# Performance work log

Measured on AMD Instinct MI355X. Metric: run time of the kernel, lower is better.

Reference implementation:

```python
import jax, jax.numpy as jnp
import numpy as np

B, T, D = 1, 1024, 4096
H, HK, DH = 32, 8, 128          # n_heads, n_kv_heads, head_dim
N_REP = H // HK                 # GQA repeat factor
RQ, RKV, RO, RFF = 64, 64, 1024, 1024
INTER = 14336
EPS = 1e-5
THETA = 10000.0


def _rms_norm(x, w):
    # LLaMA RMSNorm: x * rsqrt(mean(x^2)+eps) * w
    var = jnp.mean(x * x, axis=-1, keepdims=True)
    return x * jax.lax.rsqrt(var + EPS) * w


def _rope_cos_sin(t_len, dh):
    # _SimpleRoPE semantics: interleaved repeat of angles (repeat_interleave(2))
    evens = jnp.arange(0, dh, 2, dtype=jnp.float32)
    inv = 1.0 / (THETA ** (evens / dh))                 # [dh/2]
    t = jnp.arange(t_len, dtype=jnp.float32)
    ang = t[:, None] * inv[None, :]                     # [T, dh/2]
    ang = jnp.repeat(ang, 2, axis=-1)                   # [T, dh]
    return jnp.cos(ang), jnp.sin(ang)


def _rotate_half(x):
    # HF rotate_half: split in half along last dim
    half = x.shape[-1] // 2
    return jnp.concatenate([-x[..., half:], x[..., :half]], axis=-1)


def _apply_rope(q, k, cos, sin):
    # q,k: [B,H,T,dh]; cos/sin: [T,dh] broadcast over B,H
    c = cos[None, None]
    s = sin[None, None]
    return q * c + _rotate_half(q) * s, k * c + _rotate_half(k) * s


def _proj_per_head(x, Us, V):
    # x: [B,T,D], V: [h,r,D], Us: [h,dh,r] -> [B,h,T,dh]
    xr = jnp.einsum('btd,hrd->bthr', x, V)
    return jnp.einsum('bthr,hdr->bhtd', xr, Us)


def setup_inputs() -> dict:
    key = jax.random.key(0)
    ks = jax.random.split(key, 16)
    sc = 0.02
    inp = {
        'hidden_states': jax.random.normal(ks[0], (B, T, D), jnp.float32),
        'ln1_w': jnp.ones((D,), jnp.float32),
        'ln2_w': jnp.ones((D,), jnp.float32),
        'q_Us': jax.random.normal(ks[1], (H, DH, RQ), jnp.float32) * sc,
        'q_V': jax.random.normal(ks[2], (H, RQ, D), jnp.float32) * sc,
        'k_Us': jax.random.normal(ks[3], (HK, DH, RKV), jnp.float32) * sc,
        'k_V': jax.random.normal(ks[4], (HK, RKV, D), jnp.float32) * sc,
        'v_Us': jax.random.normal(ks[5], (HK, DH, RKV), jnp.float32) * sc,
        'v_V': jax.random.normal(ks[6], (HK, RKV, D), jnp.float32) * sc,
        'o_Us': jax.random.normal(ks[7], (D, RO), jnp.float32) * sc,
        'o_V': jax.random.normal(ks[8], (RO, H * DH), jnp.float32) * sc,
        'g_Us': jax.random.normal(ks[9], (INTER, RFF), jnp.float32) * sc,
        'g_V': jax.random.normal(ks[10], (RFF, D), jnp.float32) * sc,
        'u_Us': jax.random.normal(ks[11], (INTER, RFF), jnp.float32) * sc,
        'u_V': jax.random.normal(ks[12], (RFF, D), jnp.float32) * sc,
        'd_Us': jax.random.normal(ks[13], (D, RFF), jnp.float32) * sc,
        'd_V': jax.random.normal(ks[14], (RFF, INTER), jnp.float32) * sc,
    }
    return inp


def reference(hidden_states, ln1_w, ln2_w, q_Us, q_V, k_Us, k_V, v_Us, v_V,
              o_Us, o_V, g_Us, g_V, u_Us, u_V, d_Us, d_V):
    x = hidden_states
    # --- attention ---
    h1 = _rms_norm(x, ln1_w)
    q = _proj_per_head(h1, q_Us, q_V)            # [B,H,T,dh]
    k = _proj_per_head(h1, k_Us, k_V)            # [B,HK,T,dh]
    v = _proj_per_head(h1, v_Us, v_V)            # [B,HK,T,dh]
    cos, sin = _rope_cos_sin(T, DH)
    q, k = _apply_rope(q, k, cos, sin)
    k = jnp.repeat(k, N_REP, axis=1)             # GQA expand -> [B,H,T,dh]
    v = jnp.repeat(v, N_REP, axis=1)
    scale = 1.0 / np.sqrt(DH)
    scores = jnp.einsum('bhtd,bhsd->bhts', q, k) * scale   # [B,H,T,T]
    causal = jnp.tril(jnp.ones((T, T), bool))
    scores = jnp.where(causal[None, None], scores, jnp.float32(-1e30))
    p = jax.nn.softmax(scores, axis=-1)
    attn = jnp.einsum('bhts,bhsd->bhtd', p, v)   # [B,H,T,dh]
    attn = attn.transpose(0, 2, 1, 3).reshape(B, T, H * DH)
    # low-rank o: y = attn @ W_o^T = (attn @ V^T) @ Us^T
    y = jnp.einsum('btr,dr->btd', jnp.einsum('bte,re->btr', attn, o_V), o_Us)
    x = x + y
    # --- SwiGLU MLP with low-rank factors ---
    h2 = _rms_norm(x, ln2_w)
    g = jnp.einsum('btr,ir->bti', jnp.einsum('btd,rd->btr', h2, g_V), g_Us)
    u = jnp.einsum('btr,ir->bti', jnp.einsum('btd,rd->btr', h2, u_V), u_Us)
    hmid = jax.nn.silu(g) * u                    # [B,T,INTER]
    dn = jnp.einsum('btr,dr->btd', jnp.einsum('bti,ri->btr', hmid, d_V), d_Us)
    return x + dn
```

## Files before the change

### kernel.cpp

```cpp
#include <hip/hip_runtime.h>
#include <math.h>


typedef __bf16 bf16;
typedef __bf16 bf16x8 __attribute__((ext_vector_type(8)));
typedef __bf16 bf16x4 __attribute__((ext_vector_type(4)));
typedef float  f32x4  __attribute__((ext_vector_type(4)));

#define EPI_BF16   0
#define EPI_BF16T  1
#define EPI_F32ADD 2
#define EPI_SILU1  3
#define EPI_MUL    4
#define EPI_PART   5

__device__ __forceinline__ void gld16(const void* g, void* l) {
    __builtin_amdgcn_global_load_lds(
        (const __attribute__((address_space(1))) unsigned int*)g,
        (__attribute__((address_space(3))) unsigned int*)l, 16, 0, 0);
}

template<int EPI>
__global__ __launch_bounds__(256)
void gemm3f(const bf16* __restrict__ A, int lda, long sA,
            const float* __restrict__ B, int ldb, long sB, const float* __restrict__ B2,
            void* __restrict__ Cv, int ldc, long sC,
            const float* __restrict__ R, int Kc, int nsplit, int gx)
{
    __shared__ __align__(16) bf16  As[128 * 64];
    __shared__ __align__(16) float Bs[128 * 64];

    const int tid = threadIdx.x, lane = tid & 63, w = tid >> 6;
    const int wr = w >> 1, wc = w & 1;

    int id = blockIdx.x;
    {
        const int nwg = gridDim.x;
        int q = nwg >> 3, rr = nwg & 7;
        int xcd = id & 7, off = id >> 3;
        id = (xcd < rr ? xcd * (q + 1) : rr * (q + 1) + (xcd - rr) * q) + off;
    }
    const int bm = id % gx, bn = id / gx, bz = blockIdx.z;
    const int ks = bz % nsplit, zb = bz / nsplit;

    const float* Bp = (B2 != nullptr && zb != 0) ? B2 : B;
    const bf16*  Ab = A  + (long)zb * sA + (long)(bm * 128) * lda + (long)ks * Kc;
    const float* Bb = Bp + (long)zb * sB + (long)(bn * 128) * ldb + (long)ks * Kc;

    const int g = lane >> 4, r = lane & 15;
    f32x4 acc[4][4] = {};
    const int nt = Kc >> 6;

    for (int t = 0; t < nt; t++) {
        if (t) __syncthreads();
        const bf16*  At = Ab + t * 64;
        const float* Bt = Bb + t * 64;
        #pragma unroll
        for (int i = 0; i < 4; i++) {
            int cb = w * 256 + i * 64, ci = cb + lane;
            int row = ci >> 3, col = ((ci & 7) ^ (row & 7)) * 8;
            gld16(At + (long)row * lda + col, &As[cb * 8]);
        }
        #pragma unroll
        for (int i = 0; i < 8; i++) {
            int cb = w * 512 + i * 64, ci = cb + lane;
            int row = ci >> 4, col = ((ci & 15) ^ (row & 15)) * 4;
            gld16(Bt + (long)row * ldb + col, &Bs[cb * 4]);
        }
        __syncthreads();
        #pragma unroll
        for (int kk = 0; kk < 2; kk++) {
            bf16x8 af[4], bfr[4];
            #pragma unroll
            for (int m = 0; m < 4; m++) {
                int row = wr * 64 + m * 16 + r;
                af[m] = *(const bf16x8*)&As[row * 64 + (((kk * 4 + g) ^ (row & 7)) * 8)];
            }
            #pragma unroll
            for (int n = 0; n < 4; n++) {
                int row = wc * 64 + n * 16 + r;
                int c0 = kk * 8 + g * 2;
                f32x4 lo = *(const f32x4*)&Bs[row * 64 + (((c0    ) ^ (row & 15)) * 4)];
                f32x4 hi = *(const f32x4*)&Bs[row * 64 + (((c0 + 1) ^ (row & 15)) * 4)];
                bfr[n] = bf16x8{(bf16)lo[0], (bf16)lo[1], (bf16)lo[2], (bf16)lo[3],
                                (bf16)hi[0], (bf16)hi[1], (bf16)hi[2], (bf16)hi[3]};
            }
            #pragma unroll
            for (int m = 0; m < 4; m++)
                #pragma unroll
                for (int n = 0; n < 4; n++)
                    acc[m][n] = __builtin_amdgcn_mfma_f32_16x16x32_bf16(af[m], bfr[n], acc[m][n], 0, 0, 0);
        }
    }

    #pragma unroll
    for (int m = 0; m < 4; m++) {
        #pragma unroll
        for (int n = 0; n < 4; n++) {
            const int row0 = bm * 128 + wr * 64 + m * 16 + g * 4;
            const int col  = bn * 128 + wc * 64 + n * 16 + r;
            #pragma unroll
            for (int j = 0; j < 4; j++) {
                float v = acc[m][n][j];
                long row = row0 + j;
                if constexpr (EPI == EPI_BF16) {
                    ((bf16*)Cv)[(long)zb * sC + row * (long)ldc + col] = (bf16)v;
                } else if constexpr (EPI == EPI_BF16T) {
                    ((bf16*)Cv)[(long)zb * sC + (long)col * ldc + row] = (bf16)v;
                } else if constexpr (EPI == EPI_F32ADD) {
                    long idx = row * (long)ldc + col;
                    ((float*)Cv)[idx] = v + R[idx];
                } else if constexpr (EPI == EPI_PART) {
                    ((float*)Cv)[(long)bz * sC + row * (long)ldc + col] = v;
                } else if constexpr (EPI == EPI_SILU1) {
                    ((bf16*)Cv)[row * (long)ldc + col] = (bf16)(v / (1.f + __expf(-v)));
                } else {
                    bf16* p = &((bf16*)Cv)[row * (long)ldc + col];
                    *p = (bf16)((float)*p * v);
                }
            }
        }
    }
}

template<int EPI>
__global__ __launch_bounds__(256)
void gemm2(const bf16* __restrict__ A, int lda, long sA,
           const float* __restrict__ B, int ldb, long sB, const float* __restrict__ B2,
           void* __restrict__ Cv, int ldc, long sC,
           const float* __restrict__ R, int Kc, int nsplit)
{
    __shared__ __align__(16) bf16 As[2][128 * 64];
    __shared__ __align__(16) bf16 Bs[2][128 * 64];

    const int tid = threadIdx.x, lane = tid & 63, w = tid >> 6;
    const int wr = w >> 1, wc = w & 1;
    const int bm = blockIdx.x, bn = blockIdx.y, bz = blockIdx.z;
    const int ks = bz % nsplit, zb = bz / nsplit;

    const float* Bp = (B2 != nullptr && zb != 0) ? B2 : B;
    const bf16*  Ab = A  + (long)zb * sA + (long)(bm * 128) * lda + (long)ks * Kc;
    const float* Bb = Bp + (long)zb * sB + (long)(bn * 128) * ldb + (long)ks * Kc;

    const int g = lane >> 4, r = lane & 15;
    f32x4 acc[4][4] = {};
    const int nt = Kc >> 6;
    int cur = 0;

    {
        #pragma unroll
        for (int i = 0; i < 4; i++) {
            int cb = i * 256 + w * 64, ci = cb + lane;
            int arow = ci >> 3, acol = ((ci & 7) ^ (arow & 7)) * 8;
            gld16(Ab + (long)arow * lda + acol, &As[0][cb * 8]);
        }
        float4 fb[8];
        #pragma unroll
        for (int i = 0; i < 8; i++) {
            int p = i * 256 + tid;
            fb[i] = *(const float4*)(Bb + (long)(p >> 4) * ldb + (p & 15) * 4);
        }
        #pragma unroll
        for (int i = 0; i < 8; i++) {
            int p = i * 256 + tid, brow = p >> 4, c4 = p & 15;
            bf16x4 h = {(bf16)fb[i].x, (bf16)fb[i].y, (bf16)fb[i].z, (bf16)fb[i].w};
            *(bf16x4*)&Bs[0][brow * 64 + (((c4 >> 1) ^ (brow & 7)) * 8) + (c4 & 1) * 4] = h;
        }
    }
    __syncthreads();

    for (int t = 0; t < nt; t++) {
        float4 fb[8];
        if (t + 1 < nt) {
            const bf16* An = Ab + (t + 1) * 64;
            #pragma unroll
            for (int i = 0; i < 4; i++) {
                int cb = i * 256 + w * 64, ci = cb + lane;
                int arow = ci >> 3, acol = ((ci & 7) ^ (arow & 7)) * 8;
                gld16(An + (long)arow * lda + acol, &As[cur ^ 1][cb * 8]);
            }
            const float* Bn = Bb + (t + 1) * 64;
            #pragma unroll
            for (int i = 0; i < 8; i++) {
                int p = i * 256 + tid;
                fb[i] = *(const float4*)(Bn + (long)(p >> 4) * ldb + (p & 15) * 4);
            }
        }
        #pragma unroll
        for (int kk = 0; kk < 2; kk++) {
            bf16x8 af[4], bfr[4];
            #pragma unroll
            for (int m = 0; m < 4; m++) {
                int row = wr * 64 + m * 16 + r;
                af[m] = *(const bf16x8*)&As[cur][row * 64 + (((kk * 4 + g) ^ (row & 7)) * 8)];
            }
            #pragma unroll
            for (int n = 0; n < 4; n++) {
                int row = wc * 64 + n * 16 + r;
                bfr[n] = *(const bf16x8*)&Bs[cur][row * 64 + (((kk * 4 + g) ^ (row & 7)) * 8)];
            }
            #pragma unroll
            for (int m = 0; m < 4; m++)
                #pragma unroll
                for (int n = 0; n < 4; n++)
                    acc[m][n] = __builtin_amdgcn_mfma_f32_16x16x32_bf16(af[m], bfr[n], acc[m][n], 0, 0, 0);
        }
        if (t + 1 < nt) {
            #pragma unroll
            for (int i = 0; i < 8; i++) {
                int p = i * 256 + tid, brow = p >> 4, c4 = p & 15;
                bf16x4 h = {(bf16)fb[i].x, (bf16)fb[i].y, (bf16)fb[i].z, (bf16)fb[i].w};
                *(bf16x4*)&Bs[cur ^ 1][brow * 64 + (((c4 >> 1) ^ (brow & 7)) * 8) + (c4 & 1) * 4] = h;
            }
            __syncthreads();
            cur ^= 1;
        }
    }

    #pragma unroll
    for (int m = 0; m < 4; m++) {
        #pragma unroll
        for (int n = 0; n < 4; n++) {
            const int row0 = bm * 128 + wr * 64 + m * 16 + g * 4;
            const int col  = bn * 128 + wc * 64 + n * 16 + r;
            #pragma unroll
            for (int j = 0; j < 4; j++) {
                float v = acc[m][n][j];
                long row = row0 + j;
                if constexpr (EPI == EPI_BF16) {
                    ((bf16*)Cv)[(long)zb * sC + row * (long)ldc + col] = (bf16)v;
                } else if constexpr (EPI == EPI_BF16T) {
                    ((bf16*)Cv)[(long)zb * sC + (long)col * ldc + row] = (bf16)v;
                } else if constexpr (EPI == EPI_F32ADD) {
                    long idx = row * (long)ldc + col;
                    ((float*)Cv)[idx] = v + R[idx];
                } else if constexpr (EPI == EPI_PART) {
                    ((float*)Cv)[(long)bz * sC + row * (long)ldc + col] = v;
                } else if constexpr (EPI == EPI_SILU1) {
                    ((bf16*)Cv)[row * (long)ldc + col] = (bf16)(v / (1.f + __expf(-v)));
                } else {
                    bf16* p = &((bf16*)Cv)[row * (long)ldc + col];
                    *p = (bf16)((float)*p * v);
                }
            }
        }
    }
}

__global__ __launch_bounds__(256)
void reduce_k(const float* __restrict__ part, long pe, int np, bf16* __restrict__ out)
{
    long i = ((long)blockIdx.x * 256 + threadIdx.x) * 4;
    float4 s = *(const float4*)&part[i];
    for (int p = 1; p < np; p++) {
        float4 v = *(const float4*)&part[(long)p * pe + i];
        s.x += v.x; s.y += v.y; s.z += v.z; s.w += v.w;
    }
    bf16x4 o = {(bf16)s.x, (bf16)s.y, (bf16)s.z, (bf16)s.w};
    *(bf16x4*)&out[i] = o;
}

__global__ __launch_bounds__(256)
void rmsnorm_k(const float* __restrict__ x, const float* __restrict__ w,
               bf16* __restrict__ out)
{
    const int D = 4096;
    const long row = blockIdx.x;
    const float* xr = x + row * D;
    float4 v[4];
    float ss = 0.f;
    #pragma unroll
    for (int k = 0; k < 4; k++) {
        v[k] = *(const float4*)&xr[threadIdx.x * 4 + k * 1024];
        ss += v[k].x * v[k].x + v[k].y * v[k].y + v[k].z * v[k].z + v[k].w * v[k].w;
    }
    #pragma unroll
    for (int o = 32; o > 0; o >>= 1) ss += __shfl_down(ss, o);
    __shared__ float red[4];
    if ((threadIdx.x & 63) == 0) red[threadIdx.x >> 6] = ss;
    __syncthreads();
    float rs = rsqrtf((red[0] + red[1] + red[2] + red[3]) / D + 1e-5f);
    #pragma unroll
    for (int k = 0; k < 4; k++) {
        int i = threadIdx.x * 4 + k * 1024;
        float4 wv = *(const float4*)&w[i];
        bf16x4 o4 = {(bf16)(v[k].x * rs * wv.x), (bf16)(v[k].y * rs * wv.y),
                     (bf16)(v[k].z * rs * wv.z), (bf16)(v[k].w * rs * wv.w)};
        *(bf16x4*)&out[row * D + i] = o4;
    }
}

__global__ __launch_bounds__(256)
void rope_table_k(float* cs, float* sn)
{
    int idx = blockIdx.x * blockDim.x + threadIdx.x;
    int t = idx >> 6, i = idx & 63;
    float inv = powf(10000.0f, -(2.0f * i) / 128.0f);
    float a = (float)t * inv;
    cs[idx] = cosf(a);
    sn[idx] = sinf(a);
}

__global__ __launch_bounds__(256)
void rope_k(bf16* qk, const float* __restrict__ cs, const float* __restrict__ sn)
{
    long idx = (long)blockIdx.x * blockDim.x + threadIdx.x;
    int d = idx & 63;
    long ht = idx >> 6;
    int t = (int)(ht & 1023);
    bf16* p = qk + ht * 128;
    float x1 = (float)p[d], x2 = (float)p[d + 64];
    int i1 = d >> 1;
    float c1 = cs[t * 64 + i1],      s1 = sn[t * 64 + i1];
    float c2 = cs[t * 64 + 32 + i1], s2 = sn[t * 64 + 32 + i1];
    p[d]      = (bf16)(x1 * c1 - x2 * s1);
    p[d + 64] = (bf16)(x2 * c2 + x1 * s2);
}

__global__ __launch_bounds__(256)
void attn_k(const bf16* __restrict__ Q,
            const bf16* __restrict__ Kb,
            const bf16* __restrict__ Vt,
            bf16* __restrict__ O)
{
    const int T = 1024;
    __shared__ __align__(16) bf16 Ks[64][128];
    __shared__ __align__(16) bf16 Vs[128][64];
    __shared__ __align__(16) bf16 Ps[4][16][72];

    const int qt = blockIdx.x, h = blockIdx.y, hk = h >> 2;
    const int tid = threadIdx.x, lane = tid & 63, w = tid >> 6;
    const int g = lane >> 4, r = lane & 15;
    const int qrow0 = qt * 64 + w * 16;

    bf16x8 qf[4];
    const bf16* qp = Q + ((long)h * T + qrow0 + r) * 128;
    #pragma unroll
    for (int dc = 0; dc < 4; dc++) qf[dc] = *(const bf16x8*)(qp + dc * 32 + g * 8);

    f32x4 o_acc[8] = {};
    float m_run[4], l_run[4];
    #pragma unroll
    for (int j = 0; j < 4; j++) { m_run[j] = -1e30f; l_run[j] = 0.f; }

    const float scale = 0.08838834764831845f;
    const int kv_end = qt * 64 + 64;

    for (int kv0 = 0; kv0 < kv_end; kv0 += 64) {
        __syncthreads();
        {
            int tr = tid >> 2;
            const bf16* src = Kb + ((long)hk * T + kv0 + tr) * 128;
            #pragma unroll
            for (int q4 = 0; q4 < 4; q4++) {
                int c = (tid & 3) * 4 + q4;
                bf16x8 v = *(const bf16x8*)(src + c * 8);
                *(bf16x8*)&Ks[tr][(c ^ (tr & 7)) * 8] = v;
            }
        }
        {
            int dd = tid >> 1;
            const bf16* src = Vt + ((long)hk * 128 + dd) * T + kv0;
            #pragma unroll
            for (int q4 = 0; q4 < 4; q4++) {
                int c = (tid & 1) * 4 + q4;
                bf16x8 v = *(const bf16x8*)(src + c * 8);
                *(bf16x8*)&Vs[dd][(c ^ (dd & 7)) * 8] = v;
            }
        }
        __syncthreads();

        f32x4 s[4] = {};
        #pragma unroll
        for (int n = 0; n < 4; n++) {
            int tr = n * 16 + r;
            #pragma unroll
            for (int dc = 0; dc < 4; dc++) {
                int c = (dc * 4 + g) ^ (tr & 7);
                bf16x8 kf = *(const bf16x8*)&Ks[tr][c * 8];
                s[n] = __builtin_amdgcn_mfma_f32_16x16x32_bf16(qf[dc], kf, s[n], 0, 0, 0);
            }
        }

        #pragma unroll
        for (int j = 0; j < 4; j++) {
            int qpos = qrow0 + g * 4 + j;
            float mx = m_run[j];
            #pragma unroll
            for (int n = 0; n < 4; n++) {
                int kpos = kv0 + n * 16 + r;
                float sv = s[n][j] * scale;
                sv = (kpos <= qpos) ? sv : -1e30f;
                s[n][j] = sv;
                mx = fmaxf(mx, sv);
            }
            #pragma unroll
            for (int mask = 1; mask < 16; mask <<= 1) mx = fmaxf(mx, __shfl_xor(mx, mask));
            float corr = __expf(m_run[j] - mx);
            l_run[j] *= corr;
            #pragma unroll
            for (int db = 0; db < 8; db++) o_acc[db][j] *= corr;
            float ls = 0.f;
            #pragma unroll
            for (int n = 0; n < 4; n++) {
                float p = __expf(s[n][j] - mx);
                s[n][j] = p;
                ls += p;
            }
            #pragma unroll
            for (int mask = 1; mask < 16; mask <<= 1) ls += __shfl_xor(ls, mask);
            l_run[j] += ls;
            m_run[j] = mx;
        }

        #pragma unroll
        for (int n = 0; n < 4; n++)
            #pragma unroll
            for (int j = 0; j < 4; j++)
                Ps[w][g * 4 + j][n * 16 + r] = (bf16)s[n][j];
        __syncthreads();

        bf16x8 pf[2];
        #pragma unroll
        for (int kc = 0; kc < 2; kc++)
            pf[kc] = *(const bf16x8*)&Ps[w][r][kc * 32 + g * 8];
        #pragma unroll
        for (int db = 0; db < 8; db++) {
            #pragma unroll
            for (int kc = 0; kc < 2; kc++) {
                int dd = db * 16 + r;
                int c = (kc * 4 + g) ^ (dd & 7);
                bf16x8 vf = *(const bf16x8*)&Vs[dd][c * 8];
                o_acc[db] = __builtin_amdgcn_mfma_f32_16x16x32_bf16(pf[kc], vf, o_acc[db], 0, 0, 0);
            }
        }
    }

    #pragma unroll
    for (int db = 0; db < 8; db++) {
        #pragma unroll
        for (int j = 0; j < 4; j++) {
            int t = qrow0 + g * 4 + j;
            float v = o_acc[db][j] / l_run[j];
            O[(long)t * 4096 + h * 128 + db * 16 + r] = (bf16)v;
        }
    }
}

extern "C" void kernel_launch(void* const* d_in, const int* in_sizes, int n_in,
                              void* d_out, int out_size, void* d_ws, size_t ws_size,
                              hipStream_t stream)
{
    const float* X   = (const float*)d_in[0];
    const float* LN1 = (const float*)d_in[1];
    const float* LN2 = (const float*)d_in[2];
    const float* qUs = (const float*)d_in[3];
    const float* qV  = (const float*)d_in[4];
    const float* kUs = (const float*)d_in[5];
    const float* kV  = (const float*)d_in[6];
    const float* vUs = (const float*)d_in[7];
    const float* vV  = (const float*)d_in[8];
    const float* oUs = (const float*)d_in[9];
    const float* oV  = (const float*)d_in[10];
    const float* gUs = (const float*)d_in[11];
    const float* gV  = (const float*)d_in[12];
    const float* uUs = (const float*)d_in[13];
    const float* uV  = (const float*)d_in[14];
    const float* dUs = (const float*)d_in[15];
    const float* dV  = (const float*)d_in[16];
    float* OUT = (float*)d_out;

    char* w = (char*)d_ws;
    bf16*  h1   = (bf16*)(w + 0);
    bf16*  xrq  = (bf16*)(w + 8388608);
    bf16*  xrk  = (bf16*)(w + 12582912);
    bf16*  xrv  = (bf16*)(w + 13631488);
    bf16*  qb   = (bf16*)(w + 14680064);
    bf16*  kb   = (bf16*)(w + 23068672);
    bf16*  vt   = (bf16*)(w + 25165824);
    float* cs   = (float*)(w + 27262976);
    float* sn   = (float*)(w + 27525120);
    bf16*  att  = (bf16*)(w + 27787264);
    bf16*  r1   = (bf16*)(w + 36175872);
    bf16*  h2   = (bf16*)(w + 0);
    bf16*  gr   = (bf16*)(w + 8388608);
    bf16*  ur   = (bf16*)(w + 10485760);
    bf16*  hmid = (bf16*)(w + 12582912);
    bf16*  dr   = (bf16*)(w + 41943040);
    const size_t ARENA  = 44040192;
    const size_t PARTSZ = 33554432;
    float* part = (float*)(w + ARENA);
    const bool med = ws_size >= ARENA + PARTSZ;

    dim3 blk(256);

    if (med) {
        rmsnorm_k<<<1024, blk, 0, stream>>>(X, LN1, h1);
        gemm3f<EPI_PART><<<dim3(128,1,4), blk, 0, stream>>>(h1,4096,0, qV,4096,0,nullptr, part,2048,2097152, nullptr, 1024,4, 8);
        reduce_k<<<2048, blk, 0, stream>>>(part, 2097152, 4, xrq);
        gemm3f<EPI_PART><<<dim3(32,1,8), blk, 0, stream>>>(h1,4096,0, kV,4096,0,vV, part,512,524288, nullptr, 1024,4, 8);
        reduce_k<<<512, blk, 0, stream>>>(part,             524288, 4, xrk);
        reduce_k<<<512, blk, 0, stream>>>(part + 4L*524288, 524288, 4, xrv);

        gemm3f<EPI_BF16 ><<<dim3(8,1,32), blk, 0, stream>>>(xrq,2048,64, qUs,64,8192,nullptr, qb,128,131072, nullptr, 64,1, 8);
        gemm3f<EPI_BF16 ><<<dim3(8,1, 8), blk, 0, stream>>>(xrk, 512,64, kUs,64,8192,nullptr, kb,128,131072, nullptr, 64,1, 8);
        gemm3f<EPI_BF16T><<<dim3(8,1, 8), blk, 0, stream>>>(xrv, 512,64, vUs,64,8192,nullptr, vt,1024,131072, nullptr, 64,1, 8);
        rope_table_k<<<256, blk, 0, stream>>>(cs, sn);
        rope_k<<<8192, blk, 0, stream>>>(qb, cs, sn);
        rope_k<<<2048, blk, 0, stream>>>(kb, cs, sn);
        attn_k<<<dim3(16,32), blk, 0, stream>>>(qb, kb, vt, att);

        gemm3f<EPI_PART><<<dim3(64,1,4), blk, 0, stream>>>(att,4096,0, oV,4096,0,nullptr, part,1024,1048576, nullptr, 1024,4, 8);
        reduce_k<<<1024, blk, 0, stream>>>(part, 1048576, 4, r1);
        gemm3f<EPI_F32ADD><<<dim3(256,1,1), blk, 0, stream>>>(r1,1024,0, oUs,1024,0,nullptr, OUT,4096,0, X, 1024,1, 8);

        rmsnorm_k<<<1024, blk, 0, stream>>>(OUT, LN2, h2);
        gemm3f<EPI_PART><<<dim3(64,1,8), blk, 0, stream>>>(h2,4096,0, gV,4096,0,uV, part,1024,1048576, nullptr, 1024,4, 8);
        reduce_k<<<1024, blk, 0, stream>>>(part,              1048576, 4, gr);
        reduce_k<<<1024, blk, 0, stream>>>(part + 4L*1048576, 1048576, 4, ur);
        gemm3f<EPI_SILU1><<<dim3(896,1,1), blk, 0, stream>>>(gr,1024,0, gUs,1024,0,nullptr, hmid,14336,0, nullptr, 1024,1, 8);
        gemm3f<EPI_MUL  ><<<dim3(896,1,1), blk, 0, stream>>>(ur,1024,0, uUs,1024,0,nullptr, hmid,14336,0, nullptr, 1024,1, 8);
        gemm3f<EPI_PART><<<dim3(64,1,7), blk, 0, stream>>>(hmid,14336,0, dV,14336,0,nullptr, part,1024,1048576, nullptr, 2048,7, 8);
        reduce_k<<<1024, blk, 0, stream>>>(part, 1048576, 7, dr);
        gemm3f<EPI_F32ADD><<<dim3(256,1,1), blk, 0, stream>>>(dr,1024,0, dUs,1024,0,nullptr, OUT,4096,0, OUT, 1024,1, 8);
        return;
    }

    rmsnorm_k<<<1024, blk, 0, stream>>>(X, LN1, h1);
    gemm2<EPI_BF16><<<dim3(8,16,1), blk, 0, stream>>>(h1,4096,0, qV,4096,0,nullptr, xrq,2048,0, nullptr, 4096, 1);
    gemm2<EPI_BF16><<<dim3(8, 4,1), blk, 0, stream>>>(h1,4096,0, kV,4096,0,nullptr, xrk, 512,0, nullptr, 4096, 1);
    gemm2<EPI_BF16><<<dim3(8, 4,1), blk, 0, stream>>>(h1,4096,0, vV,4096,0,nullptr, xrv, 512,0, nullptr, 4096, 1);
    gemm2<EPI_BF16 ><<<dim3(8,1,32), blk, 0, stream>>>(xrq,2048,64, qUs,64,8192,nullptr, qb,128,131072, nullptr, 64, 1);
    gemm2<EPI_BF16 ><<<dim3(8,1, 8), blk, 0, stream>>>(xrk, 512,64, kUs,64,8192,nullptr, kb,128,131072, nullptr, 64, 1);
    gemm2<EPI_BF16T><<<dim3(8,1, 8), blk, 0, stream>>>(xrv, 512,64, vUs,64,8192,nullptr, vt,1024,131072, nullptr, 64, 1);
    rope_table_k<<<256, blk, 0, stream>>>(cs, sn);
    rope_k<<<8192, blk, 0, stream>>>(qb, cs, sn);
    rope_k<<<2048, blk, 0, stream>>>(kb, cs, sn);
    attn_k<<<dim3(16,32), blk, 0, stream>>>(qb, kb, vt, att);
    gemm2<EPI_BF16><<<dim3(8,8,1), blk, 0, stream>>>(att,4096,0, oV,4096,0,nullptr, r1,1024,0, nullptr, 4096, 1);
    gemm2<EPI_F32ADD><<<dim3(8,32,1), blk, 0, stream>>>(r1,1024,0, oUs,1024,0,nullptr, OUT,4096,0, X, 1024, 1);
    rmsnorm_k<<<1024, blk, 0, stream>>>(OUT, LN2, h2);
    gemm2<EPI_BF16><<<dim3(8,8,1), blk, 0, stream>>>(h2,4096,0, gV,4096,0,nullptr, gr,1024,0, nullptr, 4096, 1);
    gemm2<EPI_BF16><<<dim3(8,8,1), blk, 0, stream>>>(h2,4096,0, uV,4096,0,nullptr, ur,1024,0, nullptr, 4096, 1);
    gemm2<EPI_SILU1><<<dim3(8,112,1), blk, 0, stream>>>(gr,1024,0, gUs,1024,0,nullptr, hmid,14336,0, nullptr, 1024, 1);
    gemm2<EPI_MUL  ><<<dim3(8,112,1), blk, 0, stream>>>(ur,1024,0, uUs,1024,0,nullptr, hmid,14336,0, nullptr, 1024, 1);
    gemm2<EPI_BF16><<<dim3(8,8,1), blk, 0, stream>>>(hmid,14336,0, dV,14336,0,nullptr, dr,1024,0, nullptr, 14336, 1);
    gemm2<EPI_F32ADD><<<dim3(8,32,1), blk, 0, stream>>>(dr,1024,0, dUs,1024,0,nullptr, OUT,4096,0, OUT, 1024, 1);
}
```

Baseline: 526.5 us.

## Double-buffer GEMM LDS tiles with K=32 steps and async prefetch

Replaces the single-buffered K=64 GEMM main loop with a two-stage LDS pipeline that uses K=32 tiles. The next tile's global-to-LDS loads are issued before computing the current one, with a partial vmcnt wait and raw s_barrier. This overlaps memory latency with MFMA work at the same total LDS footprint, but doubles the number of barriers per K and relies on a hand-counted vmcnt value being correct.

```diff
diff --git a/kernel.cpp b/kernel.cpp
--- a/kernel.cpp
+++ b/kernel.cpp
@@ -22,13 +22,13 @@
 
 template<int EPI>
 __global__ __launch_bounds__(256)
-void gemm3f(const bf16* __restrict__ A, int lda, long sA,
-            const float* __restrict__ B, int ldb, long sB, const float* __restrict__ B2,
-            void* __restrict__ Cv, int ldc, long sC,
-            const float* __restrict__ R, int Kc, int nsplit, int gx)
-{
-    __shared__ __align__(16) bf16  As[128 * 64];
-    __shared__ __align__(16) float Bs[128 * 64];
+void gemm4(const bf16* __restrict__ A, int lda, long sA,
+           const float* __restrict__ B, int ldb, long sB, const float* __restrict__ B2,
+           void* __restrict__ Cv, int ldc, long sC,
+           const float* __restrict__ R, int Kc, int nsplit, int gx)
+{
+    __shared__ __align__(16) bf16  As[2][4096];
+    __shared__ __align__(16) float Bs[2][4096];
 
     const int tid = threadIdx.x, lane = tid & 63, w = tid >> 6;
     const int wr = w >> 1, wc = w & 1;
@@ -49,48 +49,61 @@
 
     const int g = lane >> 4, r = lane & 15;
     f32x4 acc[4][4] = {};
-    const int nt = Kc >> 6;
-
+    const int nt = Kc >> 5;
+
+    auto stage = [&](int buf, int t) {
+        const bf16*  At = Ab + t * 32;
+        const float* Bt = Bb + t * 32;
+        #pragma unroll
+        for (int i = 0; i < 2; i++) {
+            int ci = w * 128 + i * 64 + lane;
+            int s = ci >> 3, h = (ci & 7) ^ (s & 7);
+            int row = s * 2 + (h >> 2), col = (h & 3) * 8;
+            gld16(At + (long)row * lda + col, &As[buf][ci * 8]);
+        }
+        #pragma unroll
+        for (int i = 0; i < 4; i++) {
+            int ci = w * 256 + i * 64 + lane;
+            int row = ci >> 3, c = (ci & 7) ^ (row & 7);
+            gld16(Bt + (long)row * ldb + c * 4, &Bs[buf][ci * 4]);
+        }
+    };
+
+    stage(0, 0);
     for (int t = 0; t < nt; t++) {
-        if (t) __syncthreads();
-        const bf16*  At = Ab + t * 64;
-        const float* Bt = Bb + t * 64;
-        #pragma unroll
-        for (int i = 0; i < 4; i++) {
-            int cb = w * 256 + i * 64, ci = cb + lane;
-            int row = ci >> 3, col = ((ci & 7) ^ (row & 7)) * 8;
-            gld16(At + (long)row * lda + col, &As[cb * 8]);
-        }
-        #pragma unroll
-        for (int i = 0; i < 8; i++) {
-            int cb = w * 512 + i * 64, ci = cb + lane;
-            int row = ci >> 4, col = ((ci & 15) ^ (row & 15)) * 4;
-            gld16(Bt + (long)row * ldb + col, &Bs[cb * 4]);
-        }
-        __syncthreads();
-        #pragma unroll
-        for (int kk = 0; kk < 2; kk++) {
-            bf16x8 af[4], bfr[4];
-            #pragma unroll
-            for (int m = 0; m < 4; m++) {
-                int row = wr * 64 + m * 16 + r;
-                af[m] = *(const bf16x8*)&As[row * 64 + (((kk * 4 + g) ^ (row & 7)) * 8)];
-            }
-            #pragma unroll
-            for (int n = 0; n < 4; n++) {
-                int row = wc * 64 + n * 16 + r;
-                int c0 = kk * 8 + g * 2;
-                f32x4 lo = *(const f32x4*)&Bs[row * 64 + (((c0    ) ^ (row & 15)) * 4)];
-                f32x4 hi = *(const f32x4*)&Bs[row * 64 + (((c0 + 1) ^ (row & 15)) * 4)];
-                bfr[n] = bf16x8{(bf16)lo[0], (bf16)lo[1], (bf16)lo[2], (bf16)lo[3],
-                                (bf16)hi[0], (bf16)hi[1], (bf16)hi[2], (bf16)hi[3]};
-            }
-            #pragma unroll
-            for (int m = 0; m < 4; m++)
-                #pragma unroll
-                for (int n = 0; n < 4; n++)
-                    acc[m][n] = __builtin_amdgcn_mfma_f32_16x16x32_bf16(af[m], bfr[n], acc[m][n], 0, 0, 0);
-        }
+        const int cur = t & 1;
+        if (t + 1 < nt) {
+            stage(cur ^ 1, t + 1);
+            asm volatile("s_waitcnt vmcnt(6)" ::: "memory");
+        } else {
+            asm volatile("s_waitcnt vmcnt(0)" ::: "memory");
+        }
+        __builtin_amdgcn_s_barrier();
+
+        bf16x8 af[4], bfr[4];
+        #pragma unroll
+        for (int m = 0; m < 4; m++) {
+            int row = wr * 64 + m * 16 + r;
+            int s = row >> 1;
+            int slot = (((row & 1) << 2) | g) ^ (s & 7);
+            af[m] = *(const bf16x8*)&As[cur][s * 64 + slot * 8];
+        }
+        #pragma unroll
+        for (int n = 0; n < 4; n++) {
+            int row = wc * 64 + n * 16 + r;
+            int base = row * 32;
+            f32x4 lo = *(const f32x4*)&Bs[cur][base + (((2 * g    ) ^ (row & 7)) * 4)];
+            f32x4 hi = *(const f32x4*)&Bs[cur][base + (((2 * g + 1) ^ (row & 7)) * 4)];
+            bfr[n] = bf16x8{(bf16)lo[0], (bf16)lo[1], (bf16)lo[2], (bf16)lo[3],
+                            (bf16)hi[0], (bf16)hi[1], (bf16)hi[2], (bf16)hi[3]};
+        }
+        #pragma unroll
+        for (int m = 0; m < 4; m++)
+            #pragma unroll
+            for (int n = 0; n < 4; n++)
+                acc[m][n] = __builtin_amdgcn_mfma_f32_16x16x32_bf16(af[m], bfr[n], acc[m][n], 0, 0, 0);
+
+        __builtin_amdgcn_s_barrier();
     }
 
     #pragma unroll
@@ -496,33 +509,33 @@
 
     if (med) {
         rmsnorm_k<<<1024, blk, 0, stream>>>(X, LN1, h1);
-        gemm3f<EPI_PART><<<dim3(128,1,4), blk, 0, stream>>>(h1,4096,0, qV,4096,0,nullptr, part,2048,2097152, nullptr, 1024,4, 8);
+        gemm4<EPI_PART><<<dim3(128,1,4), blk, 0, stream>>>(h1,4096,0, qV,4096,0,nullptr, part,2048,2097152, nullptr, 1024,4, 8);
         reduce_k<<<2048, blk, 0, stream>>>(part, 2097152, 4, xrq);
-        gemm3f<EPI_PART><<<dim3(32,1,8), blk, 0, stream>>>(h1,4096,0, kV,4096,0,vV, part,512,524288, nullptr, 1024,4, 8);
+        gemm4<EPI_PART><<<dim3(32,1,8), blk, 0, stream>>>(h1,4096,0, kV,4096,0,vV, part,512,524288, nullptr, 1024,4, 8);
         reduce_k<<<512, blk, 0, stream>>>(part,             524288, 4, xrk);
         reduce_k<<<512, blk, 0, stream>>>(part + 4L*524288, 524288, 4, xrv);
 
-        gemm3f<EPI_BF16 ><<<dim3(8,1,32), blk, 0, stream>>>(xrq,2048,64, qUs,64,8192,nullptr, qb,128,131072, nullptr, 64,1, 8);
-        gemm3f<EPI_BF16 ><<<dim3(8,1, 8), blk, 0, stream>>>(xrk, 512,64, kUs,64,8192,nullptr, kb,128,131072, nullptr, 64,1, 8);
-        gemm3f<EPI_BF16T><<<dim3(8,1, 8), blk, 0, stream>>>(xrv, 512,64, vUs,64,8192,nullptr, vt,1024,131072, nullptr, 64,1, 8);
+        gemm4<EPI_BF16 ><<<dim3(8,1,32), blk, 0, stream>>>(xrq,2048,64, qUs,64,8192,nullptr, qb,128,131072, nullptr, 64,1, 8);
+        gemm4<EPI_BF16 ><<<dim3(8,1, 8), blk, 0, stream>>>(xrk, 512,64, kUs,64,8192,nullptr, kb,128,131072, nullptr, 64,1, 8);
+        gemm4<EPI_BF16T><<<dim3(8,1, 8), blk, 0, stream>>>(xrv, 512,64, vUs,64,8192,nullptr, vt,1024,131072, nullptr, 64,1, 8);
         rope_table_k<<<256, blk, 0, stream>>>(cs, sn);
         rope_k<<<8192, blk, 0, stream>>>(qb, cs, sn);
         rope_k<<<2048, blk, 0, stream>>>(kb, cs, sn);
         attn_k<<<dim3(16,32), blk, 0, stream>>>(qb, kb, vt, att);
 
-        gemm3f<EPI_PART><<<dim3(64,1,4), blk, 0, stream>>>(att,4096,0, oV,4096,0,nullptr, part,1024,1048576, nullptr, 1024,4, 8);
+        gemm4<EPI_PART><<<dim3(64,1,4), blk, 0, stream>>>(att,4096,0, oV,4096,0,nullptr, part,1024,1048576, nullptr, 1024,4, 8);
         reduce_k<<<1024, blk, 0, stream>>>(part, 1048576, 4, r1);
-        gemm3f<EPI_F32ADD><<<dim3(256,1,1), blk, 0, stream>>>(r1,1024,0, oUs,1024,0,nullptr, OUT,4096,0, X, 1024,1, 8);
+        gemm4<EPI_F32ADD><<<dim3(256,1,1), blk, 0, stream>>>(r1,1024,0, oUs,1024,0,nullptr, OUT,4096,0, X, 1024,1, 8);
 
         rmsnorm_k<<<1024, blk, 0, stream>>>(OUT, LN2, h2);
-        gemm3f<EPI_PART><<<dim3(64,1,8), blk, 0, stream>>>(h2,4096,0, gV,4096,0,uV, part,1024,1048576, nullptr, 1024,4, 8);
+        gemm4<EPI_PART><<<dim3(64,1,8), blk, 0, stream>>>(h2,4096,0, gV,4096,0,uV, part,1024,1048576, nullptr, 1024,4, 8);
         reduce_k<<<1024, blk, 0, stream>>>(part,              1048576, 4, gr);
         reduce_k<<<1024, blk, 0, stream>>>(part + 4L*1048576, 1048576, 4, ur);
-        gemm3f<EPI_SILU1><<<dim3(896,1,1), blk, 0, stream>>>(gr,1024,0, gUs,1024,0,nullptr, hmid,14336,0, nullptr, 1024,1, 8);
-        gemm3f<EPI_MUL  ><<<dim3(896,1,1), blk, 0, stream>>>(ur,1024,0, uUs,1024,0,nullptr, hmid,14336,0, nullptr, 1024,1, 8);
-        gemm3f<EPI_PART><<<dim3(64,1,7), blk, 0, stream>>>(hmid,14336,0, dV,14336,0,nullptr, part,1024,1048576, nullptr, 2048,7, 8);
+        gemm4<EPI_SILU1><<<dim3(896,1,1), blk, 0, stream>>>(gr,1024,0, gUs,1024,0,nullptr, hmid,14336,0, nullptr, 1024,1, 8);
+        gemm4<EPI_MUL  ><<<dim3(896,1,1), blk, 0, stream>>>(ur,1024,0, uUs,1024,0,nullptr, hmid,14336,0, nullptr, 1024,1, 8);
+        gemm4<EPI_PART><<<dim3(64,1,7), blk, 0, stream>>>(hmid,14336,0, dV,14336,0,nullptr, part,1024,1048576, nullptr, 2048,7, 8);
         reduce_k<<<1024, blk, 0, stream>>>(part, 1048576, 7, dr);
-        gemm3f<EPI_F32ADD><<<dim3(256,1,1), blk, 0, stream>>>(dr,1024,0, dUs,1024,0,nullptr, OUT,4096,0, OUT, 1024,1, 8);
+        gemm4<EPI_F32ADD><<<dim3(256,1,1), blk, 0, stream>>>(dr,1024,0, dUs,1024,0,nullptr, OUT,4096,0, OUT, 1024,1, 8);
         return;
     }
 
```

Measured after the change: 635.2 us. +20.6%, slower.

## Add 512-thread GEMM with five-stage LDS pipeline for low-rank projections

Applied to the files above, without the earlier changes.

Introduces gemm8, a 512-thread (8-wave) GEMM using 128x128 tiles with a K-step of 32 and a five-deep ring of LDS buffers, filled by direct global-to-LDS loads and synchronised through explicit vmcnt waits. All low-rank projection and up/down GEMMs in the main path now use it instead of gemm3f. The goal is to hide global memory latency with more loads in flight and more waves per block. In exchange it uses a large LDS footprint (about 120 KB per block), which limits occupancy, and adds two barriers per short K-step.

```diff
diff --git a/kernel.cpp b/kernel.cpp
--- a/kernel.cpp
+++ b/kernel.cpp
@@ -14,10 +14,127 @@
 #define EPI_MUL    4
 #define EPI_PART   5
 
+#define PDEPTH 5
+
 __device__ __forceinline__ void gld16(const void* g, void* l) {
     __builtin_amdgcn_global_load_lds(
         (const __attribute__((address_space(1))) unsigned int*)g,
         (__attribute__((address_space(3))) unsigned int*)l, 16, 0, 0);
+}
+
+template<int EPI>
+__global__ __launch_bounds__(512)
+void gemm8(const bf16* __restrict__ A, int lda, long sA,
+           const float* __restrict__ B, int ldb, long sB, const float* __restrict__ B2,
+           void* __restrict__ Cv, int ldc, long sC,
+           const float* __restrict__ R, int Kc, int nsplit, int gx)
+{
+    __shared__ __align__(16) bf16  As[PDEPTH][4096];
+    __shared__ __align__(16) float Bs[PDEPTH][4096];
+
+    const int tid = threadIdx.x, lane = tid & 63, w = tid >> 6;
+    const int wr = w >> 2, wcn = w & 3;
+
+    int id = blockIdx.x;
+    {
+        const int nwg = gridDim.x;
+        int q = nwg >> 3, rr = nwg & 7;
+        int xcd = id & 7, off = id >> 3;
+        id = (xcd < rr ? xcd * (q + 1) : rr * (q + 1) + (xcd - rr) * q) + off;
+    }
+    const int bm = id % gx, bn = id / gx, bz = blockIdx.z;
+    const int ks = bz % nsplit, zb = bz / nsplit;
+
+    const float* Bp = (B2 != nullptr && zb != 0) ? B2 : B;
+    const bf16*  Ab = A  + (long)zb * sA + (long)(bm * 128) * lda + (long)ks * Kc;
+    const float* Bb = Bp + (long)zb * sB + (long)(bn * 128) * ldb + (long)ks * Kc;
+
+    const int g = lane >> 4, r = lane & 15;
+    f32x4 acc[4][2] = {};
+    const int nt = Kc >> 5;
+
+    auto stage = [&](int buf, int t) {
+        const bf16*  At = Ab + t * 32;
+        const float* Bt = Bb + t * 32;
+        {
+            int ci = w * 64 + lane;
+            int row = ci >> 2, col = ((ci & 3) ^ (row & 3)) * 8;
+            gld16(At + (long)row * lda + col, &As[buf][w * 64 * 8]);
+        }
+        #pragma unroll
+        for (int i = 0; i < 2; i++) {
+            int cb = w * 128 + i * 64, ci = cb + lane;
+            int row = ci >> 3, c = (ci & 7) ^ (row & 7);
+            gld16(Bt + (long)row * ldb + c * 4, &Bs[buf][cb * 4]);
+        }
+    };
+
+    #pragma unroll
+    for (int d = 0; d < PDEPTH; d++) stage(d, d);
+
+    int buf = 0;
+    for (int t = 0; t < nt; t++) {
+        if (t + PDEPTH < nt) {
+            asm volatile("s_waitcnt vmcnt(12)" ::: "memory");
+        } else {
+            asm volatile("s_waitcnt vmcnt(0)" ::: "memory");
+        }
+        __builtin_amdgcn_s_barrier();
+
+        bf16x8 af[4], bfr[2];
+        #pragma unroll
+        for (int m = 0; m < 4; m++) {
+            int row = wr * 64 + m * 16 + r;
+            int slot = g ^ (row & 3);
+            af[m] = *(const bf16x8*)&As[buf][row * 32 + slot * 8];
+        }
+        #pragma unroll
+        for (int n = 0; n < 2; n++) {
+            int row = wcn * 32 + n * 16 + r;
+            f32x4 lo = *(const f32x4*)&Bs[buf][row * 32 + (((2 * g    ) ^ (row & 7)) * 4)];
+            f32x4 hi = *(const f32x4*)&Bs[buf][row * 32 + (((2 * g + 1) ^ (row & 7)) * 4)];
+            bfr[n] = bf16x8{(bf16)lo[0], (bf16)lo[1], (bf16)lo[2], (bf16)lo[3],
+                            (bf16)hi[0], (bf16)hi[1], (bf16)hi[2], (bf16)hi[3]};
+        }
+        #pragma unroll
+        for (int m = 0; m < 4; m++)
+            #pragma unroll
+            for (int n = 0; n < 2; n++)
+                acc[m][n] = __builtin_amdgcn_mfma_f32_16x16x32_bf16(af[m], bfr[n], acc[m][n], 0, 0, 0);
+
+        __builtin_amdgcn_s_barrier();
+        if (t + PDEPTH < nt) stage(buf, t + PDEPTH);
+        buf = (buf == PDEPTH - 1) ? 0 : buf + 1;
+    }
+
+    #pragma unroll
+    for (int m = 0; m < 4; m++) {
+        #pragma unroll
+        for (int n = 0; n < 2; n++) {
+            const int row0 = bm * 128 + wr * 64 + m * 16 + g * 4;
+            const int col  = bn * 128 + wcn * 32 + n * 16 + r;
+            #pragma unroll
+            for (int j = 0; j < 4; j++) {
+                float v = acc[m][n][j];
+                long row = row0 + j;
+                if constexpr (EPI == EPI_BF16) {
+                    ((bf16*)Cv)[(long)zb * sC + row * (long)ldc + col] = (bf16)v;
+                } else if constexpr (EPI == EPI_BF16T) {
+                    ((bf16*)Cv)[(long)zb * sC + (long)col * ldc + row] = (bf16)v;
+                } else if constexpr (EPI == EPI_F32ADD) {
+                    long idx = row * (long)ldc + col;
+                    ((float*)Cv)[idx] = v + R[idx];
+                } else if constexpr (EPI == EPI_PART) {
+                    ((float*)Cv)[(long)bz * sC + row * (long)ldc + col] = v;
+                } else if constexpr (EPI == EPI_SILU1) {
+                    ((bf16*)Cv)[row * (long)ldc + col] = (bf16)(v / (1.f + __expf(-v)));
+                } else {
+                    bf16* p = &((bf16*)Cv)[row * (long)ldc + col];
+                    *p = (bf16)((float)*p * v);
+                }
+            }
+        }
+    }
 }
 
 template<int EPI>
@@ -492,13 +609,13 @@
     float* part = (float*)(w + ARENA);
     const bool med = ws_size >= ARENA + PARTSZ;
 
-    dim3 blk(256);
+    dim3 blk(256), blk8(512);
 
     if (med) {
         rmsnorm_k<<<1024, blk, 0, stream>>>(X, LN1, h1);
-        gemm3f<EPI_PART><<<dim3(128,1,4), blk, 0, stream>>>(h1,4096,0, qV,4096,0,nullptr, part,2048,2097152, nullptr, 1024,4, 8);
+        gemm8<EPI_PART><<<dim3(128,1,4), blk8, 0, stream>>>(h1,4096,0, qV,4096,0,nullptr, part,2048,2097152, nullptr, 1024,4, 8);
         reduce_k<<<2048, blk, 0, stream>>>(part, 2097152, 4, xrq);
-        gemm3f<EPI_PART><<<dim3(32,1,8), blk, 0, stream>>>(h1,4096,0, kV,4096,0,vV, part,512,524288, nullptr, 1024,4, 8);
+        gemm8<EPI_PART><<<dim3(32,1,8), blk8, 0, stream>>>(h1,4096,0, kV,4096,0,vV, part,512,524288, nullptr, 1024,4, 8);
         reduce_k<<<512, blk, 0, stream>>>(part,             524288, 4, xrk);
         reduce_k<<<512, blk, 0, stream>>>(part + 4L*524288, 524288, 4, xrv);
 
@@ -510,19 +627,19 @@
         rope_k<<<2048, blk, 0, stream>>>(kb, cs, sn);
         attn_k<<<dim3(16,32), blk, 0, stream>>>(qb, kb, vt, att);
 
-        gemm3f<EPI_PART><<<dim3(64,1,4), blk, 0, stream>>>(att,4096,0, oV,4096,0,nullptr, part,1024,1048576, nullptr, 1024,4, 8);
+        gemm8<EPI_PART><<<dim3(64,1,4), blk8, 0, stream>>>(att,4096,0, oV,4096,0,nullptr, part,1024,1048576, nullptr, 1024,4, 8);
         reduce_k<<<1024, blk, 0, stream>>>(part, 1048576, 4, r1);
-        gemm3f<EPI_F32ADD><<<dim3(256,1,1), blk, 0, stream>>>(r1,1024,0, oUs,1024,0,nullptr, OUT,4096,0, X, 1024,1, 8);
+        gemm8<EPI_F32ADD><<<dim3(256,1,1), blk8, 0, stream>>>(r1,1024,0, oUs,1024,0,nullptr, OUT,4096,0, X, 1024,1, 8);
 
         rmsnorm_k<<<1024, blk, 0, stream>>>(OUT, LN2, h2);
-        gemm3f<EPI_PART><<<dim3(64,1,8), blk, 0, stream>>>(h2,4096,0, gV,4096,0,uV, part,1024,1048576, nullptr, 1024,4, 8);
+        gemm8<EPI_PART><<<dim3(64,1,8), blk8, 0, stream>>>(h2,4096,0, gV,4096,0,uV, part,1024,1048576, nullptr, 1024,4, 8);
         reduce_k<<<1024, blk, 0, stream>>>(part,              1048576, 4, gr);
         reduce_k<<<1024, blk, 0, stream>>>(part + 4L*1048576, 1048576, 4, ur);
-        gemm3f<EPI_SILU1><<<dim3(896,1,1), blk, 0, stream>>>(gr,1024,0, gUs,1024,0,nullptr, hmid,14336,0, nullptr, 1024,1, 8);
-        gemm3f<EPI_MUL  ><<<dim3(896,1,1), blk, 0, stream>>>(ur,1024,0, uUs,1024,0,nullptr, hmid,14336,0, nullptr, 1024,1, 8);
-        gemm3f<EPI_PART><<<dim3(64,1,7), blk, 0, stream>>>(hmid,14336,0, dV,14336,0,nullptr, part,1024,1048576, nullptr, 2048,7, 8);
+        gemm8<EPI_SILU1><<<dim3(896,1,1), blk8, 0, stream>>>(gr,1024,0, gUs,1024,0,nullptr, hmid,14336,0, nullptr, 1024,1, 8);
+        gemm8<EPI_MUL  ><<<dim3(896,1,1), blk8, 0, stream>>>(ur,1024,0, uUs,1024,0,nullptr, hmid,14336,0, nullptr, 1024,1, 8);
+        gemm8<EPI_PART><<<dim3(64,1,7), blk8, 0, stream>>>(hmid,14336,0, dV,14336,0,nullptr, part,1024,1048576, nullptr, 2048,7, 8);
         reduce_k<<<1024, blk, 0, stream>>>(part, 1048576, 7, dr);
-        gemm3f<EPI_F32ADD><<<dim3(256,1,1), blk, 0, stream>>>(dr,1024,0, dUs,1024,0,nullptr, OUT,4096,0, OUT, 1024,1, 8);
+        gemm8<EPI_F32ADD><<<dim3(256,1,1), blk8, 0, stream>>>(dr,1024,0, dUs,1024,0,nullptr, OUT,4096,0, OUT, 1024,1, 8);
         return;
     }
 
```

Measured after the change: 833.7 us. 58.3% more time.

## Add LDS-free register-direct GEMM for MLP gate/up/down projections

Applied to the files above, without the earlier changes.

Adds a GEMM variant that loads A (bf16) and B (fp32) fragments straight from global memory into registers, with one-step register prefetching, and skips LDS staging entirely. It is used for the three large MLP GEMMs: gate, up and down. The aim is to remove the LDS round trip and barrier overhead. The cost is uncoalesced, strided global loads with no data reuse between waves, which may raise L2/HBM traffic and register pressure.

```diff
diff --git a/kernel.cpp b/kernel.cpp
--- a/kernel.cpp
+++ b/kernel.cpp
@@ -18,6 +18,121 @@
     __builtin_amdgcn_global_load_lds(
         (const __attribute__((address_space(1))) unsigned int*)g,
         (__attribute__((address_space(3))) unsigned int*)l, 16, 0, 0);
+}
+
+template<int EPI>
+__global__ __launch_bounds__(256)
+void gemmr(const bf16* __restrict__ A, int lda, long sA,
+           const float* __restrict__ B, int ldb, long sB, const float* __restrict__ B2,
+           void* __restrict__ Cv, int ldc, long sC,
+           const float* __restrict__ R, int Kc, int nsplit, int gx)
+{
+    const int lane = threadIdx.x & 63, w = threadIdx.x >> 6;
+    const int wr = w >> 1, wc = w & 1;
+
+    int id = blockIdx.x;
+    {
+        const int nwg = gridDim.x;
+        int q = nwg >> 3, rr = nwg & 7;
+        int xcd = id & 7, off = id >> 3;
+        id = (xcd < rr ? xcd * (q + 1) : rr * (q + 1) + (xcd - rr) * q) + off;
+    }
+    const int bm = id % gx, bn = id / gx, bz = blockIdx.z;
+    const int ks = bz % nsplit, zb = bz / nsplit;
+
+    const float* Bp = (B2 != nullptr && zb != 0) ? B2 : B;
+    const int g = lane >> 4, r = lane & 15;
+
+    const bf16*  Aw = A  + (long)zb * sA + (long)(bm * 128 + wr * 64 + r) * lda + (long)ks * Kc + g * 8;
+    const float* Bw = Bp + (long)zb * sB + (long)(bn * 128 + wc * 64 + r) * ldb + (long)ks * Kc + g * 8;
+
+    f32x4 acc[4][4] = {};
+
+    bf16x8 a0, a1, a2, a3;
+    f32x4  bl0, bh0, bl1, bh1, bl2, bh2, bl3, bh3;
+
+    auto loadA = [&](int k0, bf16x8& x0, bf16x8& x1, bf16x8& x2, bf16x8& x3) {
+        x0 = *(const bf16x8*)(Aw + 0 * 16 * lda + k0);
+        x1 = *(const bf16x8*)(Aw + 1 * 16 * lda + k0);
+        x2 = *(const bf16x8*)(Aw + 2 * 16 * lda + k0);
+        x3 = *(const bf16x8*)(Aw + 3 * 16 * lda + k0);
+    };
+    auto loadB = [&](int k0, f32x4& l0, f32x4& h0, f32x4& l1, f32x4& h1,
+                     f32x4& l2, f32x4& h2, f32x4& l3, f32x4& h3) {
+        const float* b0 = Bw + 0 * 16 * ldb + k0;
+        const float* b1 = Bw + 1 * 16 * ldb + k0;
+        const float* b2 = Bw + 2 * 16 * ldb + k0;
+        const float* b3 = Bw + 3 * 16 * ldb + k0;
+        l0 = *(const f32x4*)b0; h0 = *(const f32x4*)(b0 + 4);
+        l1 = *(const f32x4*)b1; h1 = *(const f32x4*)(b1 + 4);
+        l2 = *(const f32x4*)b2; h2 = *(const f32x4*)(b2 + 4);
+        l3 = *(const f32x4*)b3; h3 = *(const f32x4*)(b3 + 4);
+    };
+
+    loadA(0, a0, a1, a2, a3);
+    loadB(0, bl0, bh0, bl1, bh1, bl2, bh2, bl3, bh3);
+
+    for (int k0 = 0; k0 < Kc; k0 += 32) {
+        bf16x8 na0, na1, na2, na3;
+        f32x4  nl0, nh0, nl1, nh1, nl2, nh2, nl3, nh3;
+        const bool more = (k0 + 32 < Kc);
+        if (more) {
+            loadA(k0 + 32, na0, na1, na2, na3);
+            loadB(k0 + 32, nl0, nh0, nl1, nh1, nl2, nh2, nl3, nh3);
+        }
+
+        bf16x8 af[4] = {a0, a1, a2, a3};
+        bf16x8 bfr[4];
+        bfr[0] = bf16x8{(bf16)bl0[0],(bf16)bl0[1],(bf16)bl0[2],(bf16)bl0[3],
+                        (bf16)bh0[0],(bf16)bh0[1],(bf16)bh0[2],(bf16)bh0[3]};
+        bfr[1] = bf16x8{(bf16)bl1[0],(bf16)bl1[1],(bf16)bl1[2],(bf16)bl1[3],
+                        (bf16)bh1[0],(bf16)bh1[1],(bf16)bh1[2],(bf16)bh1[3]};
+        bfr[2] = bf16x8{(bf16)bl2[0],(bf16)bl2[1],(bf16)bl2[2],(bf16)bl2[3],
+                        (bf16)bh2[0],(bf16)bh2[1],(bf16)bh2[2],(bf16)bh2[3]};
+        bfr[3] = bf16x8{(bf16)bl3[0],(bf16)bl3[1],(bf16)bl3[2],(bf16)bl3[3],
+                        (bf16)bh3[0],(bf16)bh3[1],(bf16)bh3[2],(bf16)bh3[3]};
+
+        #pragma unroll
+        for (int m = 0; m < 4; m++)
+            #pragma unroll
+            for (int n = 0; n < 4; n++)
+                acc[m][n] = __builtin_amdgcn_mfma_f32_16x16x32_bf16(af[m], bfr[n], acc[m][n], 0, 0, 0);
+
+        if (more) {
+            a0 = na0; a1 = na1; a2 = na2; a3 = na3;
+            bl0 = nl0; bh0 = nh0; bl1 = nl1; bh1 = nh1;
+            bl2 = nl2; bh2 = nh2; bl3 = nl3; bh3 = nh3;
+        }
+    }
+
+    #pragma unroll
+    for (int m = 0; m < 4; m++) {
+        #pragma unroll
+        for (int n = 0; n < 4; n++) {
+            const int row0 = bm * 128 + wr * 64 + m * 16 + g * 4;
+            const int col  = bn * 128 + wc * 64 + n * 16 + r;
+            #pragma unroll
+            for (int j = 0; j < 4; j++) {
+                float v = acc[m][n][j];
+                long row = row0 + j;
+                if constexpr (EPI == EPI_BF16) {
+                    ((bf16*)Cv)[(long)zb * sC + row * (long)ldc + col] = (bf16)v;
+                } else if constexpr (EPI == EPI_BF16T) {
+                    ((bf16*)Cv)[(long)zb * sC + (long)col * ldc + row] = (bf16)v;
+                } else if constexpr (EPI == EPI_F32ADD) {
+                    long idx = row * (long)ldc + col;
+                    ((float*)Cv)[idx] = v + R[idx];
+                } else if constexpr (EPI == EPI_PART) {
+                    ((float*)Cv)[(long)bz * sC + row * (long)ldc + col] = v;
+                } else if constexpr (EPI == EPI_SILU1) {
+                    ((bf16*)Cv)[row * (long)ldc + col] = (bf16)(v / (1.f + __expf(-v)));
+                } else {
+                    bf16* p = &((bf16*)Cv)[row * (long)ldc + col];
+                    *p = (bf16)((float)*p * v);
+                }
+            }
+        }
+    }
 }
 
 template<int EPI>
@@ -518,9 +633,9 @@
         gemm3f<EPI_PART><<<dim3(64,1,8), blk, 0, stream>>>(h2,4096,0, gV,4096,0,uV, part,1024,1048576, nullptr, 1024,4, 8);
         reduce_k<<<1024, blk, 0, stream>>>(part,              1048576, 4, gr);
         reduce_k<<<1024, blk, 0, stream>>>(part + 4L*1048576, 1048576, 4, ur);
-        gemm3f<EPI_SILU1><<<dim3(896,1,1), blk, 0, stream>>>(gr,1024,0, gUs,1024,0,nullptr, hmid,14336,0, nullptr, 1024,1, 8);
-        gemm3f<EPI_MUL  ><<<dim3(896,1,1), blk, 0, stream>>>(ur,1024,0, uUs,1024,0,nullptr, hmid,14336,0, nullptr, 1024,1, 8);
-        gemm3f<EPI_PART><<<dim3(64,1,7), blk, 0, stream>>>(hmid,14336,0, dV,14336,0,nullptr, part,1024,1048576, nullptr, 2048,7, 8);
+        gemmr<EPI_SILU1><<<dim3(896,1,1), blk, 0, stream>>>(gr,1024,0, gUs,1024,0,nullptr, hmid,14336,0, nullptr, 1024,1, 8);
+        gemmr<EPI_MUL  ><<<dim3(896,1,1), blk, 0, stream>>>(ur,1024,0, uUs,1024,0,nullptr, hmid,14336,0, nullptr, 1024,1, 8);
+        gemmr<EPI_PART><<<dim3(64,1,7), blk, 0, stream>>>(hmid,14336,0, dV,14336,0,nullptr, part,1024,1048576, nullptr, 2048,7, 8);
         reduce_k<<<1024, blk, 0, stream>>>(part, 1048576, 7, dr);
         gemm3f<EPI_F32ADD><<<dim3(256,1,1), blk, 0, stream>>>(dr,1024,0, dUs,1024,0,nullptr, OUT,4096,0, OUT, 1024,1, 8);
         return;
```

After: 864.5 us. 64.2% more time.
